# Kernel tuning notes

Measured on AMD Instinct MI355X. Metric: run time of the kernel, lower is better.

Reference implementation:

```python
import jax, jax.numpy as jnp
import numpy as np

N_TOKENS = 8192
D_IN = 4096
D_OUT = 4096
N_EXPERTS = 8
LORA_R = 16
LORA_ALPHA = 32.0
SCALING = LORA_ALPHA / LORA_R
MAX_THRESHOLD = 1.0 / N_EXPERTS


def setup_inputs() -> dict:
    key = jax.random.key(0)
    ks = jax.random.split(key, 7)
    s_in = 1.0 / np.sqrt(D_IN)
    s_r = 1.0 / np.sqrt(LORA_R)
    return {
        "inputs": jax.random.normal(ks[0], (N_TOKENS, D_IN), jnp.float32),
        "router_w": jax.random.uniform(ks[1], (N_EXPERTS, D_IN), jnp.float32, -s_in, s_in),
        "router_b": jax.random.uniform(ks[2], (N_EXPERTS,), jnp.float32, -s_in, s_in),
        "thr_w": jax.random.uniform(ks[3], (1, D_IN), jnp.float32, -s_in, s_in),
        "thr_b": jax.random.uniform(ks[4], (1,), jnp.float32, -s_in, s_in),
        # lora_A per expert: [E, r, D_IN]; lora_B per expert: [E, D_OUT, r]
        # (original inits lora_B to zeros; randomized here for a meaningful baseline)
        "lora_A": jax.random.uniform(ks[5], (N_EXPERTS, LORA_R, D_IN), jnp.float32, -s_in, s_in),
        "lora_B": jax.random.uniform(ks[6], (N_EXPERTS, D_OUT, LORA_R), jnp.float32, -s_r, s_r),
    }


def reference(inputs, router_w, router_b, thr_w, thr_b, lora_A, lora_B):
    # gating
    logits = inputs @ router_w.T + router_b                      # [N, E]
    gate = jax.nn.softmax(logits, axis=-1)                       # [N, E]
    thr = jax.nn.sigmoid(inputs @ thr_w.T + thr_b) * MAX_THRESHOLD  # [N, 1]
    adapted = gate - thr                                         # [N, E]
    selected = (adapted >= 0).astype(inputs.dtype)               # [N, E]
    weights = adapted * selected                                 # [N, E]
    wsum = jnp.sum(weights, axis=-1, keepdims=True)
    wsum = jnp.where(wsum == 0, jnp.ones_like(wsum), wsum)
    weights = weights / wsum                                     # [N, E]
    # experts: LoRA, linear so masked-weight 0 == not running the expert
    h = jnp.einsum('nd,erd->ner', inputs, lora_A)                # [N, E, r]
    wh = h * weights[:, :, None]                                 # [N, E, r] (tiny)
    results = jnp.einsum('ner,eor->no', wh, lora_B) * SCALING    # [N, D_OUT]
    return results
```

## Files before the change

kernel.cpp:

```cpp
#include <hip/hip_runtime.h>
#include <stdint.h>


typedef __bf16 bf16x8 __attribute__((ext_vector_type(8)));
typedef float f32x4 __attribute__((ext_vector_type(4)));
typedef __attribute__((address_space(1))) const void* gp_t;
typedef __attribute__((address_space(3))) void* lp_t;

__device__ __forceinline__ f32x4 mfma16(bf16x8 a, bf16x8 b, f32x4 c) {
  return __builtin_amdgcn_mfma_f32_16x16x32_bf16(a, b, c, 0, 0, 0);
}
__device__ __forceinline__ uint32_t bfbits(float f) {
  uint32_t u = __builtin_bit_cast(uint32_t, f);
  return (u + 0x7fffu + ((u >> 16) & 1u)) >> 16;
}
__device__ __forceinline__ uint32_t pk2(float a, float b) {
  return bfbits(a) | (bfbits(b) << 16);
}

__global__ void pack_w1p(const float* __restrict__ rw, const float* __restrict__ tw,
                         const float* __restrict__ la, uint4* __restrict__ W1p) {
  int id = blockIdx.x * 256 + threadIdx.x;
  int lane = id & 63, k32 = (id >> 6) & 127, ct = id >> 13;
  int row = ct * 16 + (lane & 15);
  int col = k32 * 32 + (lane >> 4) * 8;
  const float* src = nullptr;
  if (row < 128)      src = la + (size_t)row * 4096 + col;
  else if (row < 136) src = rw + (size_t)(row - 128) * 4096 + col;
  else if (row == 136) src = tw + col;
  float v[8];
#pragma unroll
  for (int j = 0; j < 8; ++j) v[j] = src ? src[j] : 0.f;
  uint4 u;
  u.x = pk2(v[0], v[1]); u.y = pk2(v[2], v[3]);
  u.z = pk2(v[4], v[5]); u.w = pk2(v[6], v[7]);
  W1p[(size_t)(ct * 128 + k32) * 64 + lane] = u;
}

__global__ void pack_b2p(const float* __restrict__ lb, uint4* __restrict__ B2p) {
  int id = blockIdx.x * 256 + threadIdx.x;
  int lane = id & 63, ks = (id >> 6) & 3, ct = id >> 8;
  int o = ct * 16 + (lane & 15);
  int k0 = ks * 32 + (lane >> 4) * 8;
  const float* s = lb + (size_t)(k0 >> 4) * 65536 + (size_t)o * 16 + (k0 & 15);
  uint4 u;
  u.x = pk2(s[0] * 2.f, s[1] * 2.f); u.y = pk2(s[2] * 2.f, s[3] * 2.f);
  u.z = pk2(s[4] * 2.f, s[5] * 2.f); u.w = pk2(s[6] * 2.f, s[7] * 2.f);
  B2p[(size_t)(ct * 4 + ks) * 64 + lane] = u;
}

__global__ __launch_bounds__(512, 4) void k1_gate(
    const float* __restrict__ inp, const uint4* __restrict__ W1p,
    const float* __restrict__ rb, const float* __restrict__ tb,
    unsigned short* __restrict__ wh) {
  __shared__ __align__(16) char smem[38656];
  char* const Ab  = smem;
  char* const whl = smem + 33024;
  float* const scores = (float*)(smem + 37120);
  float* const wgt    = (float*)(smem + 38144);

  const int t = threadIdx.x;
  const int lane = t & 63;
  const int w = t >> 6;
  const int l15 = lane & 15;
  const int lq = lane >> 4;
  const int n0 = blockIdx.x * 16;
  const int rx = (l15 & 7) << 4;

  const int srow = t >> 5;
  const float* ap = inp + (size_t)(n0 + srow) * 4096 + (t & 31) * 4;
  const int sx = (srow & 7) << 4;

  f32x4 accO = {};
  f32x4 acc8 = {};
  float4 av[4];

#pragma unroll
  for (int j = 0; j < 4; ++j) av[j] = *(const float4*)(ap + j * 128);
  {
    char* d2 = Ab + srow * 1024;
#pragma unroll
    for (int j = 0; j < 4; ++j) {
      uint2 u; u.x = pk2(av[j].x, av[j].y); u.y = pk2(av[j].z, av[j].w);
      *(uint2*)(d2 + (((t & 31) * 8 + j * 256) ^ sx)) = u;
    }
  }
  __syncthreads();

  for (int c = 0; c < 8; ++c) {
    const int buf = c & 1;
    if (c < 7) {
#pragma unroll
      for (int j = 0; j < 4; ++j)
        av[j] = *(const float4*)(ap + (c + 1) * 512 + j * 128);
    }
    const char* A0 = Ab + buf * 16384;
    const uint4* wown = W1p + (size_t)(w * 128 + c * 16) * 64 + lane;
#pragma unroll
    for (int ks = 0; ks < 16; ++ks) {
      bf16x8 b = __builtin_bit_cast(bf16x8, wown[(size_t)ks * 64]);
      bf16x8 a = *(const bf16x8*)(A0 + l15 * 1024 + ((ks * 64 + lq * 16) ^ rx));
      accO = mfma16(a, b, accO);
    }
    const uint4* w8 = W1p + (size_t)(8 * 128 + c * 16) * 64 + lane;
#pragma unroll
    for (int ii = 0; ii < 2; ++ii) {
      const int ks8 = w + ii * 8;
      bf16x8 b8 = __builtin_bit_cast(bf16x8, w8[(size_t)ks8 * 64]);
      bf16x8 a = *(const bf16x8*)(A0 + l15 * 1024 + ((ks8 * 64 + lq * 16) ^ rx));
      acc8 = mfma16(a, b8, acc8);
    }
    if (c < 7) {
      char* d2 = Ab + (buf ^ 1) * 16384 + srow * 1024;
#pragma unroll
      for (int j = 0; j < 4; ++j) {
        uint2 u; u.x = pk2(av[j].x, av[j].y); u.y = pk2(av[j].z, av[j].w);
        *(uint2*)(d2 + (((t & 31) * 8 + j * 256) ^ sx)) = u;
      }
    }
    __syncthreads();
  }

  *(f32x4*)(Ab + (size_t)(w * 64 + lane) * 16) = acc8;
  __syncthreads();
  if (t < 256) {
    const int l = t >> 2, r_ = t & 3;
    float s = 0.f;
#pragma unroll
    for (int w2 = 0; w2 < 8; ++w2)
      s += ((const float*)Ab)[(w2 * 64 + l) * 4 + r_];
    scores[((l >> 4) * 4 + r_) * 16 + (l & 15)] = s;
  }
  __syncthreads();
  if (t < 16) {
    float l_[9];
#pragma unroll
    for (int e = 0; e < 9; ++e) l_[e] = scores[t * 16 + e];
    float mx = -3.4e38f;
#pragma unroll
    for (int e = 0; e < 8; ++e) { l_[e] += rb[e]; mx = fmaxf(mx, l_[e]); }
    float g[8], s = 0.f;
#pragma unroll
    for (int e = 0; e < 8; ++e) { g[e] = __expf(l_[e] - mx); s += g[e]; }
    const float thr = 0.125f / (1.f + __expf(-(l_[8] + tb[0])));
    const float inv = 1.f / s;
    float wv[8], ws = 0.f;
#pragma unroll
    for (int e = 0; e < 8; ++e) { wv[e] = fmaxf(g[e] * inv - thr, 0.f); ws += wv[e]; }
    const float wn = (ws == 0.f) ? 1.f : ws;
#pragma unroll
    for (int e = 0; e < 8; ++e) wgt[t * 8 + e] = wv[e] / wn;
  }
  __syncthreads();
#pragma unroll
  for (int r_ = 0; r_ < 4; ++r_) {
    const int tok = lq * 4 + r_;
    *(unsigned short*)(whl + tok * 256 + (((w * 16 + l15) * 2) ^ ((tok & 7) << 4))) =
        (unsigned short)bfbits(accO[r_] * wgt[tok * 8 + w]);
  }
  __syncthreads();
  if (t < 256) {
    const int row = t >> 4, seg = t & 15;
    ((uint4*)(wh + (size_t)(n0 + row) * 128))[seg] =
        ((const uint4*)(whl + row * 256))[seg];
  }
}

__global__ __launch_bounds__(512, 4) void k2_out(
    const unsigned short* __restrict__ wh, const uint4* __restrict__ B2p,
    float* __restrict__ out) {
  __shared__ __align__(16) char Bl[32768];
  __shared__ __align__(16) char Ob[32768];
  const int t = threadIdx.x, lane = t & 63, w = t >> 6;
  const int l15 = lane & 15, lq = lane >> 4;
  const int bid = blockIdx.x;
  const int tokg = bid >> 5, colg = bid & 31;
  const int n0 = tokg * 256, c0 = colg * 128;

  {
    const uint4* src = B2p + (size_t)(colg * 32) * 64;
#pragma unroll
    for (int i = 0; i < 4; ++i)
      __builtin_amdgcn_global_load_lds((gp_t)(const void*)(src + i * 512 + t),
          (lp_t)(void*)(Bl + (i * 512 + w * 64) * 16), 16, 0, 0);
  }
  __syncthreads();

  const int srow = t >> 3, sseg = t & 7;
  const int swz = (srow & 7) << 4;

#pragma unroll
  for (int tt = 0; tt < 2; ++tt) {
    const int tok = n0 + tt * 128 + w * 16 + l15;
    bf16x8 pa[4];
    const uint4* whu = (const uint4*)wh + (size_t)tok * 16;
#pragma unroll
    for (int ks = 0; ks < 4; ++ks)
      pa[ks] = __builtin_bit_cast(bf16x8, whu[(ks * 4 + lq) ^ (l15 & 7)]);
    f32x4 acc[8] = {};
#pragma unroll
    for (int ct = 0; ct < 8; ++ct)
#pragma unroll
      for (int ks = 0; ks < 4; ++ks) {
        bf16x8 b = *(const bf16x8*)(Bl + (size_t)((ct * 4 + ks) * 64 + lane) * 16);
        acc[ct] = mfma16(b, pa[ks], acc[ct]);
      }
#pragma unroll
    for (int sr = 0; sr < 2; ++sr) {
      if ((w >> 2) == sr) {
        const int tl = (w & 3) * 16 + l15;
        char* d = Ob + tl * 512;
#pragma unroll
        for (int ct = 0; ct < 8; ++ct)
          *(f32x4*)(d + ((ct * 64 + lq * 16) ^ ((tl & 7) << 4))) = acc[ct];
      }
      __syncthreads();
      {
        float* op = out + (size_t)(n0 + tt * 128 + sr * 64 + srow) * 4096 + c0 + sseg * 4;
#pragma unroll
        for (int j = 0; j < 4; ++j) {
          f32x4 v = *(const f32x4*)(Ob + srow * 512 + ((sseg * 16 + j * 128) ^ swz));
          __builtin_nontemporal_store(v, (f32x4*)(op + j * 32));
        }
      }
      __syncthreads();
    }
  }
}

extern "C" void kernel_launch(void* const* d_in, const int* in_sizes, int n_in,
                              void* d_out, int out_size, void* d_ws, size_t ws_size,
                              hipStream_t stream) {
  (void)in_sizes; (void)n_in; (void)out_size; (void)ws_size;
  const float* inp      = (const float*)d_in[0];
  const float* router_w = (const float*)d_in[1];
  const float* router_b = (const float*)d_in[2];
  const float* thr_w    = (const float*)d_in[3];
  const float* thr_b    = (const float*)d_in[4];
  const float* lora_A   = (const float*)d_in[5];
  const float* lora_B   = (const float*)d_in[6];
  float* out = (float*)d_out;

  char* ws = (char*)d_ws;
  uint4*          W1p = (uint4*)ws;
  uint4*          B2p = (uint4*)(ws + 1179648);
  unsigned short* wh  = (unsigned short*)(ws + 1179648 + 1048576);

  pack_w1p<<<288, 256, 0, stream>>>(router_w, thr_w, lora_A, W1p);
  pack_b2p<<<256, 256, 0, stream>>>(lora_B, B2p);
  k1_gate<<<512, 512, 0, stream>>>(inp, W1p, router_b, thr_b, wh);
  k2_out<<<1024, 512, 0, stream>>>(wh, B2p, out);
}
```

Before: 78.77 us.

## Widen gate kernel to 32-token tiles with split-K across 16 waves

The gate/LoRA-A kernel now processes 32 tokens per block with 1024 threads. The 16 waves split the K dimension into two halves, each wave group handling 8 column tiles, and the partial sums are reduced through shared memory afterwards. Each weight fragment loaded from global memory now feeds two MFMAs, which halves weight traffic per token and cuts the loop to 4 stages. In exchange the kernel uses more LDS, has fewer blocks (256) and adds a cross-wave reduction, so occupancy and latency hiding may suffer.

```diff
diff --git a/kernel.cpp b/kernel.cpp
--- a/kernel.cpp
+++ b/kernel.cpp
@@ -49,90 +49,122 @@
   B2p[(size_t)(ct * 4 + ks) * 64 + lane] = u;
 }
 
-__global__ __launch_bounds__(512, 4) void k1_gate(
+__global__ __launch_bounds__(1024) void k1_gate(
     const float* __restrict__ inp, const uint4* __restrict__ W1p,
     const float* __restrict__ rb, const float* __restrict__ tb,
     unsigned short* __restrict__ wh) {
-  __shared__ __align__(16) char smem[38656];
+  __shared__ __align__(16) char smem[76288];
   char* const Ab  = smem;
-  char* const whl = smem + 33024;
-  float* const scores = (float*)(smem + 37120);
-  float* const wgt    = (float*)(smem + 38144);
+  char* const whl = smem + 65536;
+  float* const scores = (float*)(smem + 73728);
+  float* const wgt    = (float*)(smem + 75776);
 
   const int t = threadIdx.x;
   const int lane = t & 63;
   const int w = t >> 6;
+  const int kg = w >> 3;
+  const int ct_ = w & 7;
   const int l15 = lane & 15;
   const int lq = lane >> 4;
-  const int n0 = blockIdx.x * 16;
+  const int n0 = blockIdx.x * 32;
   const int rx = (l15 & 7) << 4;
 
   const int srow = t >> 5;
-  const float* ap = inp + (size_t)(n0 + srow) * 4096 + (t & 31) * 4;
+  const int scf = t & 31;
+  const float* ap = inp + (size_t)(n0 + srow) * 4096 + scf * 4;
   const int sx = (srow & 7) << 4;
 
-  f32x4 accO = {};
-  f32x4 acc8 = {};
-  float4 av[4];
-
-#pragma unroll
-  for (int j = 0; j < 4; ++j) av[j] = *(const float4*)(ap + j * 128);
-  {
-    char* d2 = Ab + srow * 1024;
+  f32x4 accO[2] = {}, acc8[2] = {};
+  float4 av[2][4];
+
+  const uint4* wown = W1p + (size_t)(ct_ * 128) * 64 + lane;
+  const uint4* w8b  = W1p + (size_t)(8 * 128) * 64 + lane;
+
+#pragma unroll
+  for (int g = 0; g < 2; ++g)
+#pragma unroll
+    for (int j = 0; j < 4; ++j)
+      av[g][j] = *(const float4*)(ap + (size_t)(g * 4) * 512 + j * 128);
+#pragma unroll
+  for (int g = 0; g < 2; ++g) {
+    char* d2 = Ab + g * 32768 + srow * 1024;
 #pragma unroll
     for (int j = 0; j < 4; ++j) {
-      uint2 u; u.x = pk2(av[j].x, av[j].y); u.y = pk2(av[j].z, av[j].w);
-      *(uint2*)(d2 + (((t & 31) * 8 + j * 256) ^ sx)) = u;
-    }
-  }
-  __syncthreads();
-
-  for (int c = 0; c < 8; ++c) {
-    const int buf = c & 1;
-    if (c < 7) {
-#pragma unroll
-      for (int j = 0; j < 4; ++j)
-        av[j] = *(const float4*)(ap + (c + 1) * 512 + j * 128);
-    }
-    const char* A0 = Ab + buf * 16384;
-    const uint4* wown = W1p + (size_t)(w * 128 + c * 16) * 64 + lane;
+      uint2 u; u.x = pk2(av[g][j].x, av[g][j].y); u.y = pk2(av[g][j].z, av[g][j].w);
+      *(uint2*)(d2 + ((scf * 8 + j * 256) ^ sx)) = u;
+    }
+  }
+  __syncthreads();
+
+  for (int c = 0; c < 4; ++c) {
+    if (c < 3) {
+#pragma unroll
+      for (int g = 0; g < 2; ++g)
+#pragma unroll
+        for (int j = 0; j < 4; ++j)
+          av[g][j] = *(const float4*)(ap + (size_t)(g * 4 + c + 1) * 512 + j * 128);
+    }
+    const int ck = kg * 4 + c;
+    const char* A0 = Ab + kg * 32768;
 #pragma unroll
     for (int ks = 0; ks < 16; ++ks) {
-      bf16x8 b = __builtin_bit_cast(bf16x8, wown[(size_t)ks * 64]);
-      bf16x8 a = *(const bf16x8*)(A0 + l15 * 1024 + ((ks * 64 + lq * 16) ^ rx));
-      accO = mfma16(a, b, accO);
-    }
-    const uint4* w8 = W1p + (size_t)(8 * 128 + c * 16) * 64 + lane;
+      bf16x8 b = __builtin_bit_cast(bf16x8, wown[(size_t)(ck * 16 + ks) * 64]);
+      bf16x8 a0 = *(const bf16x8*)(A0 + l15 * 1024 + ((ks * 64 + lq * 16) ^ rx));
+      bf16x8 a1 = *(const bf16x8*)(A0 + (16 + l15) * 1024 + ((ks * 64 + lq * 16) ^ rx));
+      accO[0] = mfma16(a0, b, accO[0]);
+      accO[1] = mfma16(a1, b, accO[1]);
+    }
 #pragma unroll
     for (int ii = 0; ii < 2; ++ii) {
-      const int ks8 = w + ii * 8;
-      bf16x8 b8 = __builtin_bit_cast(bf16x8, w8[(size_t)ks8 * 64]);
-      bf16x8 a = *(const bf16x8*)(A0 + l15 * 1024 + ((ks8 * 64 + lq * 16) ^ rx));
-      acc8 = mfma16(a, b8, acc8);
-    }
-    if (c < 7) {
-      char* d2 = Ab + (buf ^ 1) * 16384 + srow * 1024;
-#pragma unroll
-      for (int j = 0; j < 4; ++j) {
-        uint2 u; u.x = pk2(av[j].x, av[j].y); u.y = pk2(av[j].z, av[j].w);
-        *(uint2*)(d2 + (((t & 31) * 8 + j * 256) ^ sx)) = u;
+      const int ks8 = ct_ + ii * 8;
+      bf16x8 b8 = __builtin_bit_cast(bf16x8, w8b[(size_t)(ck * 16 + ks8) * 64]);
+      bf16x8 a0 = *(const bf16x8*)(A0 + l15 * 1024 + ((ks8 * 64 + lq * 16) ^ rx));
+      bf16x8 a1 = *(const bf16x8*)(A0 + (16 + l15) * 1024 + ((ks8 * 64 + lq * 16) ^ rx));
+      acc8[0] = mfma16(a0, b8, acc8[0]);
+      acc8[1] = mfma16(a1, b8, acc8[1]);
+    }
+    if (c < 3) {
+      __syncthreads();
+#pragma unroll
+      for (int g = 0; g < 2; ++g) {
+        char* d2 = Ab + g * 32768 + srow * 1024;
+#pragma unroll
+        for (int j = 0; j < 4; ++j) {
+          uint2 u; u.x = pk2(av[g][j].x, av[g][j].y); u.y = pk2(av[g][j].z, av[g][j].w);
+          *(uint2*)(d2 + ((scf * 8 + j * 256) ^ sx)) = u;
+        }
       }
     }
     __syncthreads();
   }
 
-  *(f32x4*)(Ab + (size_t)(w * 64 + lane) * 16) = acc8;
-  __syncthreads();
-  if (t < 256) {
-    const int l = t >> 2, r_ = t & 3;
-    float s = 0.f;
-#pragma unroll
-    for (int w2 = 0; w2 < 8; ++w2)
-      s += ((const float*)Ab)[(w2 * 64 + l) * 4 + r_];
-    scores[((l >> 4) * 4 + r_) * 16 + (l & 15)] = s;
-  }
-  __syncthreads();
-  if (t < 16) {
+  *(f32x4*)(Ab + (size_t)((w * 2 + 0) * 64 + lane) * 16) = accO[0];
+  *(f32x4*)(Ab + (size_t)((w * 2 + 1) * 64 + lane) * 16) = accO[1];
+  *(f32x4*)(Ab + 32768 + (size_t)((w * 2 + 0) * 64 + lane) * 16) = acc8[0];
+  *(f32x4*)(Ab + 32768 + (size_t)((w * 2 + 1) * 64 + lane) * 16) = acc8[1];
+  __syncthreads();
+  f32x4 hO[2] = {};
+  if (w < 8) {
+#pragma unroll
+    for (int tt = 0; tt < 2; ++tt) {
+      f32x4 x = *(const f32x4*)(Ab + (size_t)((w * 2 + tt) * 64 + lane) * 16);
+      f32x4 y = *(const f32x4*)(Ab + (size_t)(((w + 8) * 2 + tt) * 64 + lane) * 16);
+#pragma unroll
+      for (int r_ = 0; r_ < 4; ++r_) hO[tt][r_] = x[r_] + y[r_];
+    }
+  }
+  if (t < 512) {
+    const int tok = t >> 4, col = t & 15;
+    const int tt = tok >> 4, lq_ = (tok >> 2) & 3, r_ = tok & 3;
+    float sv = 0.f;
+#pragma unroll
+    for (int w2 = 0; w2 < 16; ++w2)
+      sv += *(const float*)(Ab + 32768 +
+            (size_t)((w2 * 2 + tt) * 64 + lq_ * 16 + col) * 16 + r_ * 4);
+    scores[tok * 16 + col] = sv;
+  }
+  __syncthreads();
+  if (t < 32) {
     float l_[9];
 #pragma unroll
     for (int e = 0; e < 9; ++e) l_[e] = scores[t * 16 + e];
@@ -152,14 +184,18 @@
     for (int e = 0; e < 8; ++e) wgt[t * 8 + e] = wv[e] / wn;
   }
   __syncthreads();
-#pragma unroll
-  for (int r_ = 0; r_ < 4; ++r_) {
-    const int tok = lq * 4 + r_;
-    *(unsigned short*)(whl + tok * 256 + (((w * 16 + l15) * 2) ^ ((tok & 7) << 4))) =
-        (unsigned short)bfbits(accO[r_] * wgt[tok * 8 + w]);
-  }
-  __syncthreads();
-  if (t < 256) {
+  if (w < 8) {
+#pragma unroll
+    for (int tt = 0; tt < 2; ++tt)
+#pragma unroll
+      for (int r_ = 0; r_ < 4; ++r_) {
+        const int tok = tt * 16 + lq * 4 + r_;
+        *(unsigned short*)(whl + tok * 256 + (((w * 16 + l15) * 2) ^ ((tok & 7) << 4))) =
+            (unsigned short)bfbits(hO[tt][r_] * wgt[tok * 8 + w]);
+      }
+  }
+  __syncthreads();
+  if (t < 512) {
     const int row = t >> 4, seg = t & 15;
     ((uint4*)(wh + (size_t)(n0 + row) * 128))[seg] =
         ((const uint4*)(whl + row * 256))[seg];
@@ -248,6 +284,6 @@
 
   pack_w1p<<<288, 256, 0, stream>>>(router_w, thr_w, lora_A, W1p);
   pack_b2p<<<256, 256, 0, stream>>>(lora_B, B2p);
-  k1_gate<<<512, 512, 0, stream>>>(inp, W1p, router_b, thr_b, wh);
+  k1_gate<<<256, 1024, 0, stream>>>(inp, W1p, router_b, thr_b, wh);
   k2_out<<<1024, 512, 0, stream>>>(wh, B2p, out);
 }
```

Result: faster. 71.03 us (-9.8%).
